# Kernel optimization log

Hardware: AMD Instinct MI355X
Metric: run time of the kernel (lower is better)

The kernel has to match this reference:

```python
import jax, jax.numpy as jnp
import numpy as np

N_NODES = 50000
N_EDGES = 1280000
N_GRAPHS = 64
IN_CH = 6
HID = 64
SLOPE = 0.2  # LeakyReLU negative slope


def _lrelu(x):
    return jax.nn.leaky_relu(x, SLOPE)


def _edge_conv(x, src, dst, W1, b1, W2, b2):
    # PyG EdgeConv: message = nn([x_i, x_j - x_i]); x_i = x[dst], x_j = x[src]; max-aggr onto dst
    xi = x[dst]                                   # [E, F]
    m = jnp.concatenate([xi, x[src] - xi], -1)    # [E, 2F]
    h = _lrelu(_lrelu(m @ W1 + b1) @ W2 + b2)     # [E, H]
    agg = jax.ops.segment_max(h, dst, num_segments=N_NODES)
    return jnp.where(jnp.isneginf(agg), 0.0, agg)  # nodes with no in-edges -> 0


def setup_inputs() -> dict:
    key = jax.random.key(0)
    ks = jax.random.split(key, 12)
    glorot = lambda k, fi, fo: jax.random.normal(k, (fi, fo), jnp.float32) * np.sqrt(2.0 / (fi + fo))
    x = jax.random.normal(ks[0], (N_NODES, IN_CH), jnp.float32)
    edge_index = jax.random.randint(ks[1], (2, N_EDGES), 0, N_NODES, jnp.int64 if jax.config.x64_enabled else jnp.int32)
    batch = jnp.sort(jax.random.randint(ks[2], (N_NODES,), 0, N_GRAPHS))
    return {
        "x": x, "edge_index": edge_index, "batch": batch,
        "W1": glorot(ks[3], 2 * IN_CH, HID), "b1": jnp.zeros((HID,), jnp.float32),
        "W2": glorot(ks[4], HID, HID),       "b2": jnp.zeros((HID,), jnp.float32),
        "W3": glorot(ks[5], 2 * HID, HID),   "b3": jnp.zeros((HID,), jnp.float32),
        "W4": glorot(ks[6], HID, HID),       "b4": jnp.zeros((HID,), jnp.float32),
        "Wc1": glorot(ks[7], 2 * HID, HID),  "bc1": jnp.zeros((HID,), jnp.float32),
        "Wc2": glorot(ks[8], HID, 1),        "bc2": jnp.zeros((1,), jnp.float32),
    }


def reference(x, edge_index, batch, W1, b1, W2, b2, W3, b3, W4, b4, Wc1, bc1, Wc2, bc2):
    src, dst = edge_index[0], edge_index[1]
    h = _edge_conv(x, src, dst, W1, b1, W2, b2)   # [N, H]
    h = _edge_conv(h, src, dst, W3, b3, W4, b4)   # [N, H]
    # global mean + max pool per graph
    cnt = jax.ops.segment_sum(jnp.ones((N_NODES,), h.dtype), batch, num_segments=N_GRAPHS)
    mean_p = jax.ops.segment_sum(h, batch, num_segments=N_GRAPHS) / jnp.clip(cnt, 1.0)[:, None]
    max_p = jax.ops.segment_max(h, batch, num_segments=N_GRAPHS)
    max_p = jnp.where(jnp.isneginf(max_p), 0.0, max_p)
    g = jnp.concatenate([mean_p, max_p], -1)      # [G, 2H]
    logits = _lrelu(g @ Wc1 + bc1) @ Wc2 + bc2    # dropout is identity at inference
    return logits.squeeze(-1)                      # [G]
```

## Files before the change

### kernel.cpp

```cpp
#include <hip/hip_runtime.h>
#include <hip/hip_bf16.h>

#define SLOPE 0.2f
#define NPB 64
#define CAP 2048
#define SUBCAP 384
#define MAXBUCK 1024
#define EPB 4096
#define XF1B 512
#define PPARTS 16

typedef _Float16 f16x8  __attribute__((ext_vector_type(8)));
typedef float    f32x4  __attribute__((ext_vector_type(4)));
typedef unsigned u32;
typedef unsigned u32x4  __attribute__((ext_vector_type(4)));

__device__ __forceinline__ float lrelu(float v) { return fmaxf(v, SLOPE * v); }

__device__ __forceinline__ f16x8 lrelu8(f16x8 v) {
    f16x8 s = v * (_Float16)SLOPE;
#if __has_builtin(__builtin_elementwise_max)
    return __builtin_elementwise_max(v, s);
#else
    f16x8 r;
#pragma unroll
    for (int i = 0; i < 8; ++i) r[i] = v[i] > s[i] ? v[i] : s[i];
    return r;
#endif
}

__device__ __forceinline__ void split_f16(float v, _Float16& h, _Float16& l) {
    h = (_Float16)v;
    l = (_Float16)(v - (float)h);
}
__device__ __forceinline__ u32 pack_f16(_Float16 a, _Float16 b) {
    return (u32)__builtin_bit_cast(unsigned short, a) |
           ((u32)__builtin_bit_cast(unsigned short, b) << 16);
}

__global__ void __launch_bounds__(256) scatter_xform1_kernel(
    const int* __restrict__ srcI, const int* __restrict__ dstI,
    int* __restrict__ cursor, u32* __restrict__ pairW,
    int E, int nNodes, int nBuck, int nCntB,
    const float* __restrict__ x,
    const float* __restrict__ W1, const float* __restrict__ b1,
    _Float16* __restrict__ Ph, _Float16* __restrict__ Qh)
{
    if (blockIdx.x < nCntB) {
        __shared__ int cnt4[4][MAXBUCK];
        __shared__ int base[MAXBUCK];
        const int tid = threadIdx.x;
        const int wv  = tid >> 6;
        const int j   = blockIdx.x & 7;
        const int e0 = blockIdx.x * EPB;
        const int e1 = min(e0 + EPB, E);
        const int n4 = (e1 - e0) >> 2;
        const int4* d4 = (const int4*)(dstI + e0);
        const int4* s4 = (const int4*)(srcI + e0);

        for (int b = tid; b < nBuck; b += 256) {
            cnt4[0][b] = 0; cnt4[1][b] = 0; cnt4[2][b] = 0; cnt4[3][b] = 0;
        }
        __syncthreads();
        int* mycnt = cnt4[wv];
        for (int i = tid; i < n4; i += 256) {
            const int4 d = d4[i];
            atomicAdd(&mycnt[d.x >> 6], 1);
            atomicAdd(&mycnt[d.y >> 6], 1);
            atomicAdd(&mycnt[d.z >> 6], 1);
            atomicAdd(&mycnt[d.w >> 6], 1);
        }
        for (int e = e0 + (n4 << 2) + tid; e < e1; e += 256)
            atomicAdd(&mycnt[dstI[e] >> 6], 1);
        __syncthreads();
        for (int b = tid; b < nBuck; b += 256) {
            const int c = (cnt4[0][b] + cnt4[1][b]) + (cnt4[2][b] + cnt4[3][b]);
            base[b] = (c > 0)
                ? ((b * 8 + j) * SUBCAP + min(atomicAdd(&cursor[b * 8 + j], c), SUBCAP))
                : 0;
        }
        __syncthreads();
        for (int b = tid; b < nBuck; b += 256) cnt4[0][b] = 0;
        __syncthreads();
        int* scnt = cnt4[0];
        for (int i = tid; i < n4; i += 256) {
            const int4 d = d4[i];
            const int4 s = s4[i];
            {
                const int b = d.x >> 6;
                const int loc = atomicAdd(&scnt[b], 1);
                pairW[min(base[b] + loc, (b * 8 + j + 1) * SUBCAP - 1)] =
                    ((u32)s.x << 6) | (u32)(d.x & (NPB - 1));
            }
            {
                const int b = d.y >> 6;
                const int loc = atomicAdd(&scnt[b], 1);
                pairW[min(base[b] + loc, (b * 8 + j + 1) * SUBCAP - 1)] =
                    ((u32)s.y << 6) | (u32)(d.y & (NPB - 1));
            }
            {
                const int b = d.z >> 6;
                const int loc = atomicAdd(&scnt[b], 1);
                pairW[min(base[b] + loc, (b * 8 + j + 1) * SUBCAP - 1)] =
                    ((u32)s.z << 6) | (u32)(d.z & (NPB - 1));
            }
            {
                const int b = d.w >> 6;
                const int loc = atomicAdd(&scnt[b], 1);
                pairW[min(base[b] + loc, (b * 8 + j + 1) * SUBCAP - 1)] =
                    ((u32)s.w << 6) | (u32)(d.w & (NPB - 1));
            }
        }
        for (int e = e0 + (n4 << 2) + tid; e < e1; e += 256) {
            const int d = dstI[e];
            const int b = d >> 6;
            const int loc = atomicAdd(&scnt[b], 1);
            pairW[min(base[b] + loc, (b * 8 + j + 1) * SUBCAP - 1)] =
                ((u32)srcI[e] << 6) | (u32)(d & (NPB - 1));
        }
        return;
    }
    const int lane = threadIdx.x & 63;
    const int wave = ((blockIdx.x - nCntB) * 256 + threadIdx.x) >> 6;
    const int nw   = (XF1B * 256) >> 6;

    float wd[6], wb[6];
#pragma unroll
    for (int r = 0; r < 6; ++r) {
        wb[r] = W1[(6 + r) * 64 + lane];
        wd[r] = W1[r * 64 + lane] - wb[r];
    }
    const float bb = b1[lane];
    for (int i = wave; i < nNodes; i += nw) {
        const float* xr = x + (size_t)i * 6;
        float p = bb, q = 0.f;
#pragma unroll
        for (int r = 0; r < 6; ++r) {
            float xv = xr[r];
            p = fmaf(xv, wd[r], p);
            q = fmaf(xv, wb[r], q);
        }
        Ph[(size_t)i * 64 + lane] = (_Float16)p;
        Qh[(size_t)i * 64 + lane] = (_Float16)q;
    }
}

__global__ void __launch_bounds__(256) bucket_sort_kernel(
    const u32* __restrict__ pairW, const int* __restrict__ cursor,
    int2* __restrict__ rowInfo, int* __restrict__ sortedSrc, int nNodes)
{
    __shared__ u32 pairLds[CAP];
    __shared__ int nodeCnt4[4][NPB];
    __shared__ int nodeCur4[4][NPB];
    __shared__ int wcS[8];
    __shared__ int wBase[9];
    const int b   = blockIdx.x;
    const int n0  = b * NPB;
    const int n1  = min(n0 + NPB, nNodes);
    const int tid = threadIdx.x;
    const int wv  = tid >> 6;

    if (tid < NPB) {
        nodeCnt4[0][tid] = 0; nodeCnt4[1][tid] = 0;
        nodeCnt4[2][tid] = 0; nodeCnt4[3][tid] = 0;
    }
    if (tid < 8) wcS[tid] = min(cursor[b * 8 + tid], SUBCAP);
    __syncthreads();
    if (tid == 0) {
        int acc = 0;
#pragma unroll
        for (int jj = 0; jj < 8; ++jj) { wBase[jj] = acc; acc += wcS[jj]; }
        wBase[8] = acc;
    }
    __syncthreads();

#pragma unroll
    for (int jj = 0; jj < 8; ++jj) {
        const int w0 = (b * 8 + jj) * SUBCAP;
        const int wc = wcS[jj];
        const int d0 = wBase[jj];
        const int nv = wc >> 2;
        const u32x4* p4 = (const u32x4*)(pairW + w0);
        for (int i = tid; i < nv; i += 256) {
            const u32x4 v = p4[i];
            pairLds[d0 + i * 4 + 0] = v[0];
            pairLds[d0 + i * 4 + 1] = v[1];
            pairLds[d0 + i * 4 + 2] = v[2];
            pairLds[d0 + i * 4 + 3] = v[3];
        }
        for (int i = (nv << 2) + tid; i < wc; i += 256)
            pairLds[d0 + i] = pairW[w0 + i];
    }
    __syncthreads();

    const int total = wBase[8];
    for (int i = tid; i < total; i += 256)
        atomicAdd(&nodeCnt4[wv][pairLds[i] & (NPB - 1)], 1);
    __syncthreads();
    if (tid < 64) {
        const int c0 = nodeCnt4[0][tid], c1 = nodeCnt4[1][tid];
        const int c2 = nodeCnt4[2][tid], c3 = nodeCnt4[3][tid];
        const int c = (c0 + c1) + (c2 + c3);
        int inc = c;
#pragma unroll
        for (int off = 1; off < 64; off <<= 1) {
            int t = __shfl_up(inc, off);
            if (tid >= off) inc += t;
        }
        const int st = b * CAP + inc - c;
        nodeCur4[0][tid] = st;
        nodeCur4[1][tid] = st + c0;
        nodeCur4[2][tid] = st + c0 + c1;
        nodeCur4[3][tid] = st + c0 + c1 + c2;
        if (tid < n1 - n0) rowInfo[n0 + tid] = make_int2(st, c);
    }
    __syncthreads();
    for (int i = tid; i < total; i += 256) {
        const u32 w = pairLds[i];
        const int pos = atomicAdd(&nodeCur4[wv][w & (NPB - 1)], 1);
        sortedSrc[pos] = (int)(w >> 6);
    }
}

__global__ void __launch_bounds__(256) node_xform2_mfma_kernel(
    const _Float16* __restrict__ B1h,
    const float* __restrict__ W3, const float* __restrict__ b3,
    _Float16* __restrict__ Ph, _Float16* __restrict__ Qh, int nNodes)
{
    __shared__ u32x4 wlds[32][64];

    const int tid  = threadIdx.x;
    const int lane = tid & 63;
    const int cn   = lane & 15;
    const int q    = lane >> 4;
    const int wv   = tid >> 6;
    const int wave = (blockIdx.x * 256 + tid) >> 6;
    const int nw   = (gridDim.x * 256) >> 6;

#pragma unroll
    for (int i = 0; i < 8; ++i) {
        const int f    = wv + i * 4;
        const int isLo = f >> 4;
        const int g    = f & 15;
        const int nt   = g >> 1;
        const int ks   = g & 1;
        const int col  = (nt & 3) * 16 + cn;
        u32x4 d;
#pragma unroll
        for (int p = 0; p < 4; ++p) {
            const int k0 = ks * 32 + q * 8 + 2 * p;
            float w0, w1;
            if (nt < 4) {
                w0 = W3[k0 * 64 + col]       - W3[(64 + k0) * 64 + col];
                w1 = W3[(k0 + 1) * 64 + col] - W3[(64 + k0 + 1) * 64 + col];
            } else {
                w0 = W3[(64 + k0) * 64 + col];
                w1 = W3[(64 + k0 + 1) * 64 + col];
            }
            _Float16 h0, l0, h1, l1;
            split_f16(w0, h0, l0);
            split_f16(w1, h1, l1);
            d[p] = isLo ? pack_f16(l0, l1) : pack_f16(h0, h1);
        }
        wlds[f][lane] = d;
    }
    float bcv[4];
#pragma unroll
    for (int nt = 0; nt < 4; ++nt) bcv[nt] = b3[nt * 16 + cn];
    __syncthreads();

    const int nGrp = (nNodes + 15) >> 4;
    for (int t = wave; t < nGrp; t += nw) {
        const int n0 = t << 4;
        const int rA = min(n0 + cn, nNodes - 1);
        const f16x8* Arow = (const f16x8*)(B1h + (size_t)rA * 64);
        const f16x8 A0 = Arow[q];
        const f16x8 A1 = Arow[4 + q];

        f32x4 acc0, acc1, acc2, acc3, acc4, acc5, acc6, acc7;
#define NT_TILE(ACC, NT, INI)                                                  \
        {                                                                      \
            const f16x8 wh0 = __builtin_bit_cast(f16x8, wlds[(NT) * 2][lane]); \
            const f16x8 wh1 = __builtin_bit_cast(f16x8, wlds[(NT) * 2 + 1][lane]); \
            const f16x8 wl0 = __builtin_bit_cast(f16x8, wlds[16 + (NT) * 2][lane]); \
            const f16x8 wl1 = __builtin_bit_cast(f16x8, wlds[16 + (NT) * 2 + 1][lane]); \
            f32x4 a_; a_[0] = a_[1] = a_[2] = a_[3] = (INI);                   \
            a_ = __builtin_amdgcn_mfma_f32_16x16x32_f16(A0, wl0, a_, 0, 0, 0); \
            a_ = __builtin_amdgcn_mfma_f32_16x16x32_f16(A0, wh0, a_, 0, 0, 0); \
            a_ = __builtin_amdgcn_mfma_f32_16x16x32_f16(A1, wl1, a_, 0, 0, 0); \
            a_ = __builtin_amdgcn_mfma_f32_16x16x32_f16(A1, wh1, a_, 0, 0, 0); \
            ACC = a_;                                                          \
        }
        NT_TILE(acc0, 0, bcv[0]); NT_TILE(acc1, 1, bcv[1]);
        NT_TILE(acc2, 2, bcv[2]); NT_TILE(acc3, 3, bcv[3]);
        NT_TILE(acc4, 4, 0.0f);   NT_TILE(acc5, 5, 0.0f);
        NT_TILE(acc6, 6, 0.0f);   NT_TILE(acc7, 7, 0.0f);
#undef NT_TILE

        const int rowLim = nNodes - n0;
#pragma unroll
        for (int j = 0; j < 4; ++j) {
            const int r = 4 * q + j;
            if (r < rowLim) {
                _Float16* Pr = Ph + (size_t)(n0 + r) * 64;
                _Float16* Qr = Qh + (size_t)(n0 + r) * 64;
                Pr[cn]      = (_Float16)acc0[j];
                Pr[16 + cn] = (_Float16)acc1[j];
                Pr[32 + cn] = (_Float16)acc2[j];
                Pr[48 + cn] = (_Float16)acc3[j];
                Qr[cn]      = (_Float16)acc4[j];
                Qr[16 + cn] = (_Float16)acc5[j];
                Qr[32 + cn] = (_Float16)acc6[j];
                Qr[48 + cn] = (_Float16)acc7[j];
            }
        }
    }
}

__global__ void __launch_bounds__(256) edge_agg_mfma_kernel(
    const _Float16* __restrict__ Ph, const _Float16* __restrict__ Qh,
    const int2* __restrict__ rowInfo, const int* __restrict__ sortedSrc,
    const float* __restrict__ W, const float* __restrict__ b,
    _Float16* __restrict__ outB, int nNodes)
{
    __shared__ u32x4 wlds[16][64];

    const int tid  = threadIdx.x;
    const int lane = tid & 63;
    const int cn   = lane & 15;
    const int q    = lane >> 4;
    const int wv   = tid >> 6;
    const int wave = (blockIdx.x * 256 + tid) >> 6;
    const int nw   = (gridDim.x * 256) >> 6;

#pragma unroll
    for (int i = 0; i < 4; ++i) {
        const int f    = wv + i * 4;
        const int isLo = f >> 3;
        const int g    = f & 7;
        const int nt   = g >> 1;
        const int ks   = g & 1;
        u32x4 d;
#pragma unroll
        for (int p = 0; p < 4; ++p) {
            float w0 = W[(ks * 32 + q * 8 + 2 * p)     * 64 + nt * 16 + cn];
            float w1 = W[(ks * 32 + q * 8 + 2 * p + 1) * 64 + nt * 16 + cn];
            _Float16 h0, l0, h1, l1;
            split_f16(w0, h0, l0);
            split_f16(w1, h1, l1);
            d[p] = isLo ? pack_f16(l0, l1) : pack_f16(h0, h1);
        }
        wlds[f][lane] = d;
    }
    float bc[4];
#pragma unroll
    for (int nt = 0; nt < 4; ++nt) bc[nt] = b[nt * 16 + cn];
    __syncthreads();

    const u32 nClamp = (u32)(nNodes - 1);
    const int nPairs = (nNodes + 1) >> 1;

    for (int t = wave; t < nPairs; t += nw) {
        const int n1 = 2 * t;
        const int n2 = 2 * t + 1;
        const bool has2 = (n2 < nNodes);

        const int2 ri1 = rowInfo[n1];
        const int2 ri2 = has2 ? rowInfo[n2] : make_int2(ri1.x, 0);
        const int rs1  = __builtin_amdgcn_readfirstlane(ri1.x);
        const int deg1 = __builtin_amdgcn_readfirstlane(ri1.y);
        const int rs2  = __builtin_amdgcn_readfirstlane(ri2.x);
        const int deg2 = __builtin_amdgcn_readfirstlane(ri2.y);
        const int d1c = max(deg1, 1) - 1;
        const int d2c = max(deg2, 1) - 1;

        const f16x8* P1 = (const f16x8*)(Ph + (size_t)n1 * 64);
        const f16x8* P2 = (const f16x8*)(Ph + (size_t)(has2 ? n2 : n1) * 64);
        const f16x8 p1A = P1[q], p1B = P1[4 + q];
        const f16x8 p2A = P2[q], p2B = P2[4 + q];

        float m10 = -INFINITY, m11 = -INFINITY, m12 = -INFINITY, m13 = -INFINITY;
        float m20 = -INFINITY, m21 = -INFINITY, m22 = -INFINITY, m23 = -INFINITY;

        const int gmax = max(deg1, deg2);
        for (int g0 = 0; g0 < gmax; g0 += 32) {
            u32 sA1 = (u32)sortedSrc[rs1 + min(g0 + cn,      d1c)];
            u32 sB1 = (u32)sortedSrc[rs1 + min(g0 + 16 + cn, d1c)];
            u32 sA2 = (u32)sortedSrc[rs2 + min(g0 + cn,      d2c)];
            u32 sB2 = (u32)sortedSrc[rs2 + min(g0 + 16 + cn, d2c)];
            sA1 = min(sA1, nClamp); sB1 = min(sB1, nClamp);
            sA2 = min(sA2, nClamp); sB2 = min(sB2, nClamp);
            const f16x8* QA1 = (const f16x8*)(Qh + (size_t)sA1 * 64);
            const f16x8* QB1 = (const f16x8*)(Qh + (size_t)sB1 * 64);
            const f16x8* QA2 = (const f16x8*)(Qh + (size_t)sA2 * 64);
            const f16x8* QB2 = (const f16x8*)(Qh + (size_t)sB2 * 64);
            const f16x8 qA1a = QA1[q], qA1b = QA1[4 + q];
            const f16x8 qB1a = QB1[q], qB1b = QB1[4 + q];
            const f16x8 qA2a = QA2[q], qA2b = QA2[4 + q];
            const f16x8 qB2a = QB2[q], qB2b = QB2[4 + q];

            if (g0 < deg1) {
                const f16x8 A00 = lrelu8(p1A + qA1a);
                const f16x8 A01 = lrelu8(p1B + qA1b);
                const f16x8 A10 = lrelu8(p1A + qB1a);
                const f16x8 A11 = lrelu8(p1B + qB1b);
#pragma unroll
                for (int nt = 0; nt < 4; ++nt) {
                    const f16x8 wh0 = __builtin_bit_cast(f16x8, wlds[nt * 2][lane]);
                    const f16x8 wh1 = __builtin_bit_cast(f16x8, wlds[nt * 2 + 1][lane]);
                    const f16x8 wl0 = __builtin_bit_cast(f16x8, wlds[8 + nt * 2][lane]);
                    const f16x8 wl1 = __builtin_bit_cast(f16x8, wlds[8 + nt * 2 + 1][lane]);
                    f32x4 a; a[0] = a[1] = a[2] = a[3] = bc[nt];
                    a = __builtin_amdgcn_mfma_f32_16x16x32_f16(A00, wl0, a, 0, 0, 0);
                    a = __builtin_amdgcn_mfma_f32_16x16x32_f16(A00, wh0, a, 0, 0, 0);
                    a = __builtin_amdgcn_mfma_f32_16x16x32_f16(A01, wl1, a, 0, 0, 0);
                    a = __builtin_amdgcn_mfma_f32_16x16x32_f16(A01, wh1, a, 0, 0, 0);
                    f32x4 c; c[0] = c[1] = c[2] = c[3] = bc[nt];
                    c = __builtin_amdgcn_mfma_f32_16x16x32_f16(A10, wl0, c, 0, 0, 0);
                    c = __builtin_amdgcn_mfma_f32_16x16x32_f16(A10, wh0, c, 0, 0, 0);
                    c = __builtin_amdgcn_mfma_f32_16x16x32_f16(A11, wl1, c, 0, 0, 0);
                    c = __builtin_amdgcn_mfma_f32_16x16x32_f16(A11, wh1, c, 0, 0, 0);
                    float m = (nt == 0) ? m10 : (nt == 1) ? m11 : (nt == 2) ? m12 : m13;
                    m = fmaxf(m, fmaxf(fmaxf(a[0], a[1]), fmaxf(a[2], a[3])));
                    m = fmaxf(m, fmaxf(fmaxf(c[0], c[1]), fmaxf(c[2], c[3])));
                    if (nt == 0) m10 = m; else if (nt == 1) m11 = m;
                    else if (nt == 2) m12 = m; else m13 = m;
                }
            }
            if (g0 < deg2) {
                const f16x8 A00 = lrelu8(p2A + qA2a);
                const f16x8 A01 = lrelu8(p2B + qA2b);
                const f16x8 A10 = lrelu8(p2A + qB2a);
                const f16x8 A11 = lrelu8(p2B + qB2b);
#pragma unroll
                for (int nt = 0; nt < 4; ++nt) {
                    const f16x8 wh0 = __builtin_bit_cast(f16x8, wlds[nt * 2][lane]);
                    const f16x8 wh1 = __builtin_bit_cast(f16x8, wlds[nt * 2 + 1][lane]);
                    const f16x8 wl0 = __builtin_bit_cast(f16x8, wlds[8 + nt * 2][lane]);
                    const f16x8 wl1 = __builtin_bit_cast(f16x8, wlds[8 + nt * 2 + 1][lane]);
                    f32x4 a; a[0] = a[1] = a[2] = a[3] = bc[nt];
                    a = __builtin_amdgcn_mfma_f32_16x16x32_f16(A00, wl0, a, 0, 0, 0);
                    a = __builtin_amdgcn_mfma_f32_16x16x32_f16(A00, wh0, a, 0, 0, 0);
                    a = __builtin_amdgcn_mfma_f32_16x16x32_f16(A01, wl1, a, 0, 0, 0);
                    a = __builtin_amdgcn_mfma_f32_16x16x32_f16(A01, wh1, a, 0, 0, 0);
                    f32x4 c; c[0] = c[1] = c[2] = c[3] = bc[nt];
                    c = __builtin_amdgcn_mfma_f32_16x16x32_f16(A10, wl0, c, 0, 0, 0);
                    c = __builtin_amdgcn_mfma_f32_16x16x32_f16(A10, wh0, c, 0, 0, 0);
                    c = __builtin_amdgcn_mfma_f32_16x16x32_f16(A11, wl1, c, 0, 0, 0);
                    c = __builtin_amdgcn_mfma_f32_16x16x32_f16(A11, wh1, c, 0, 0, 0);
                    float m = (nt == 0) ? m20 : (nt == 1) ? m21 : (nt == 2) ? m22 : m23;
                    m = fmaxf(m, fmaxf(fmaxf(a[0], a[1]), fmaxf(a[2], a[3])));
                    m = fmaxf(m, fmaxf(fmaxf(c[0], c[1]), fmaxf(c[2], c[3])));
                    if (nt == 0) m20 = m; else if (nt == 1) m21 = m;
                    else if (nt == 2) m22 = m; else m23 = m;
                }
            }
        }

        m10 = fmaxf(m10, __shfl_xor(m10, 16)); m10 = fmaxf(m10, __shfl_xor(m10, 32));
        m11 = fmaxf(m11, __shfl_xor(m11, 16)); m11 = fmaxf(m11, __shfl_xor(m11, 32));
        m12 = fmaxf(m12, __shfl_xor(m12, 16)); m12 = fmaxf(m12, __shfl_xor(m12, 32));
        m13 = fmaxf(m13, __shfl_xor(m13, 16)); m13 = fmaxf(m13, __shfl_xor(m13, 32));
        float sel1 = (q < 2) ? ((q == 0) ? m10 : m11) : ((q == 2) ? m12 : m13);
        outB[(size_t)n1 * 64 + q * 16 + cn] =
            (_Float16)((deg1 > 0) ? lrelu(sel1) : 0.0f);

        if (has2) {
            m20 = fmaxf(m20, __shfl_xor(m20, 16)); m20 = fmaxf(m20, __shfl_xor(m20, 32));
            m21 = fmaxf(m21, __shfl_xor(m21, 16)); m21 = fmaxf(m21, __shfl_xor(m21, 32));
            m22 = fmaxf(m22, __shfl_xor(m22, 16)); m22 = fmaxf(m22, __shfl_xor(m22, 32));
            m23 = fmaxf(m23, __shfl_xor(m23, 16)); m23 = fmaxf(m23, __shfl_xor(m23, 32));
            float sel2 = (q < 2) ? ((q == 0) ? m20 : m21) : ((q == 2) ? m22 : m23);
            outB[(size_t)n2 * 64 + q * 16 + cn] =
                (_Float16)((deg2 > 0) ? lrelu(sel2) : 0.0f);
        }
    }
}

__device__ __forceinline__ int lower_bound_i(const int* __restrict__ a, int n, int key)
{
    int lo = 0, hi = n;
    while (lo < hi) {
        int mid = (lo + hi) >> 1;
        if (a[mid] < key) lo = mid + 1; else hi = mid;
    }
    return lo;
}

__global__ void __launch_bounds__(256) pool_kernel(
    const _Float16* __restrict__ Bh, const int* __restrict__ batch,
    float* __restrict__ gpart, int nNodes)
{
    const int gid  = blockIdx.x / PPARTS;
    const int part = blockIdx.x % PPARTS;
    const int c    = threadIdx.x & 63;
    const int wid  = threadIdx.x >> 6;

    const int s = lower_bound_i(batch, nNodes, gid);
    const int e = lower_bound_i(batch, nNodes, gid + 1);
    const int len = e - s;
    const int ps = s + (len * part) / PPARTS;
    const int pe = s + (len * (part + 1)) / PPARTS;

    float sum = 0.f, mx = -INFINITY;
    for (int n = ps + wid; n < pe; n += 4) {
        float v = (float)Bh[(size_t)n * 64 + c];
        sum += v;
        mx = fmaxf(mx, v);
    }
    __shared__ float ssum[4][64];
    __shared__ float smax[4][64];
    ssum[wid][c] = sum;
    smax[wid][c] = mx;
    __syncthreads();
    if (wid == 0) {
        sum = (ssum[0][c] + ssum[1][c]) + (ssum[2][c] + ssum[3][c]);
        mx  = fmaxf(fmaxf(smax[0][c], smax[1][c]), fmaxf(smax[2][c], smax[3][c]));
        float* row = gpart + (size_t)blockIdx.x * 132;
        row[c]      = sum;
        row[64 + c] = mx;
        if (c == 0) row[128] = (float)(pe - ps);
    }
}

__global__ void __launch_bounds__(64) cls_kernel(
    const float* __restrict__ gpart,
    const float* __restrict__ Wc1, const float* __restrict__ bc1,
    const float* __restrict__ Wc2, const float* __restrict__ bc2,
    float* __restrict__ out)
{
    __shared__ float g[128];
    const int gid = blockIdx.x;
    const int c   = threadIdx.x;

    float s = 0.f, m = -INFINITY, cnt = 0.f;
#pragma unroll
    for (int p = 0; p < PPARTS; ++p) {
        const float* row = gpart + (size_t)(gid * PPARTS + p) * 132;
        s += row[c];
        m = fmaxf(m, row[64 + c]);
        cnt += row[128];
    }
    g[c]      = s / fmaxf(cnt, 1.0f);
    g[64 + c] = (cnt > 0.f) ? m : 0.0f;
    __syncthreads();

    float t = bc1[c];
#pragma unroll 8
    for (int k = 0; k < 128; ++k) t = fmaf(g[k], Wc1[k * 64 + c], t);
    t = lrelu(t);
    float p = t * Wc2[c];
#pragma unroll
    for (int off = 32; off > 0; off >>= 1) p += __shfl_down(p, off);
    if (c == 0) out[gid] = p + bc2[0];
}

static inline size_t align_up(size_t v, size_t a) { return (v + a - 1) & ~(a - 1); }

extern "C" void kernel_launch(void* const* d_in, const int* in_sizes, int n_in,
                              void* d_out, int out_size, void* d_ws, size_t ws_size,
                              hipStream_t stream)
{
    const float* x     = (const float*)d_in[0];
    const int*   ei    = (const int*)d_in[1];
    const int*   batch = (const int*)d_in[2];
    const float* W1  = (const float*)d_in[3];
    const float* b1  = (const float*)d_in[4];
    const float* W2  = (const float*)d_in[5];
    const float* b2  = (const float*)d_in[6];
    const float* W3  = (const float*)d_in[7];
    const float* b3  = (const float*)d_in[8];
    const float* W4  = (const float*)d_in[9];
    const float* b4  = (const float*)d_in[10];
    const float* Wc1 = (const float*)d_in[11];
    const float* bc1 = (const float*)d_in[12];
    const float* Wc2 = (const float*)d_in[13];
    const float* bc2 = (const float*)d_in[14];
    float* out = (float*)d_out;

    const int nNodes  = in_sizes[0] / 6;
    const int E       = in_sizes[1] / 2;
    const int nGraphs = out_size;
    const int* srcI = ei;
    const int* dstI = ei + E;
    const int nBuck = (nNodes + NPB - 1) / NPB;
    const int nCntB = (E + EPB - 1) / EPB;

    char* wsp = (char*)d_ws;
    size_t off = 0;
    int*  cursor    = (int*)(wsp + off);   off = align_up(off + (size_t)MAXBUCK * 8 * 4, 256);
    int2* rowInfo   = (int2*)(wsp + off);  off = align_up(off + (size_t)nNodes * 8, 256);
    int*  sortedSrc = (int*)(wsp + off);   off = align_up(off + (size_t)nBuck * CAP * 4, 256);
    u32*  pairW     = (u32*)(wsp + off);   off = align_up(off + (size_t)nBuck * 8 * SUBCAP * 4, 256);
    const size_t nFeat = (size_t)nNodes * 64;
    _Float16* Ph   = (_Float16*)(wsp + off);  off = align_up(off + nFeat * 2, 256);
    _Float16* Qh   = (_Float16*)(wsp + off);  off = align_up(off + nFeat * 2, 256);
    _Float16* B1h  = (_Float16*)(wsp + off);  off = align_up(off + nFeat * 2, 256);
    _Float16* B2h  = (_Float16*)(wsp + off);  off = align_up(off + nFeat * 2, 256);
    float*    gpart= (float*)(wsp + off);     off = align_up(off + (size_t)nGraphs * PPARTS * 132 * 4, 256);
    (void)ws_size;

    (void)hipMemsetAsync(cursor, 0, (size_t)nBuck * 8 * 4, stream);
    scatter_xform1_kernel<<<nCntB + XF1B, 256, 0, stream>>>(
        srcI, dstI, cursor, pairW, E, nNodes, nBuck, nCntB, x, W1, b1, Ph, Qh);
    bucket_sort_kernel<<<nBuck, 256, 0, stream>>>(pairW, cursor, rowInfo,
                                                  sortedSrc, nNodes);

    edge_agg_mfma_kernel<<<2048, 256, 0, stream>>>(Ph, Qh, rowInfo, sortedSrc,
                                                   W2, b2, B1h, nNodes);
    const int nGrp   = (nNodes + 15) >> 4;
    const int xf2Blk = (nGrp + 3) >> 2;
    node_xform2_mfma_kernel<<<xf2Blk, 256, 0, stream>>>(B1h, W3, b3, Ph, Qh,
                                                        nNodes);
    edge_agg_mfma_kernel<<<2048, 256, 0, stream>>>(Ph, Qh, rowInfo, sortedSrc,
                                                   W4, b4, B2h, nNodes);

    pool_kernel<<<nGraphs * PPARTS, 256, 0, stream>>>(B2h, batch, gpart, nNodes);
    cls_kernel<<<nGraphs, 64, 0, stream>>>(gpart, Wc1, bc1, Wc2, bc2, out);
}
```

Measured before the change: 261.4 us.

## Precompute padded first-32 neighbor lists to hoist gathers ahead of rowInfo dependency

The bucket sort now stages the sorted sources in LDS and also writes a fixed 32-entry padded neighbor list per node (fixedSrc). The edge aggregation kernel loads the first 32 neighbor indices and their Q rows directly, without waiting on rowInfo, so the dependent load chain (rowInfo -> sortedSrc -> Qh) is shortened for the first chunk, which covers most nodes given an average degree of about 26. This costs an extra 6.4MB index array write plus extra LDS in the sort kernel, and duplicates the first-chunk compute code.

```diff
diff --git a/kernel.cpp b/kernel.cpp
--- a/kernel.cpp
+++ b/kernel.cpp
@@ -147,11 +147,15 @@
 
 __global__ void __launch_bounds__(256) bucket_sort_kernel(
     const u32* __restrict__ pairW, const int* __restrict__ cursor,
-    int2* __restrict__ rowInfo, int* __restrict__ sortedSrc, int nNodes)
+    int2* __restrict__ rowInfo, int* __restrict__ sortedSrc,
+    int* __restrict__ fixedSrc, int nNodes)
 {
     __shared__ u32 pairLds[CAP];
+    __shared__ u32 sortLds[CAP];
     __shared__ int nodeCnt4[4][NPB];
     __shared__ int nodeCur4[4][NPB];
+    __shared__ int nodeSt[NPB];
+    __shared__ int nodeDg[NPB];
     __shared__ int wcS[8];
     __shared__ int wBase[9];
     const int b   = blockIdx.x;
@@ -207,18 +211,34 @@
             int t = __shfl_up(inc, off);
             if (tid >= off) inc += t;
         }
-        const int st = b * CAP + inc - c;
-        nodeCur4[0][tid] = st;
-        nodeCur4[1][tid] = st + c0;
-        nodeCur4[2][tid] = st + c0 + c1;
-        nodeCur4[3][tid] = st + c0 + c1 + c2;
-        if (tid < n1 - n0) rowInfo[n0 + tid] = make_int2(st, c);
+        const int stl = inc - c;
+        nodeSt[tid] = stl;
+        nodeDg[tid] = c;
+        nodeCur4[0][tid] = stl;
+        nodeCur4[1][tid] = stl + c0;
+        nodeCur4[2][tid] = stl + c0 + c1;
+        nodeCur4[3][tid] = stl + c0 + c1 + c2;
+        if (tid < n1 - n0) rowInfo[n0 + tid] = make_int2(b * CAP + stl, c);
     }
     __syncthreads();
     for (int i = tid; i < total; i += 256) {
         const u32 w = pairLds[i];
         const int pos = atomicAdd(&nodeCur4[wv][w & (NPB - 1)], 1);
-        sortedSrc[pos] = (int)(w >> 6);
+        sortLds[pos] = w >> 6;
+    }
+    __syncthreads();
+    for (int i = tid; i < total; i += 256)
+        sortedSrc[b * CAP + i] = (int)sortLds[i];
+    const int nValid = n1 - n0;
+    for (int idx = tid; idx < NPB * 32; idx += 256) {
+        const int r = idx >> 5;
+        const int i = idx & 31;
+        if (r < nValid) {
+            const int dg = nodeDg[r];
+            const u32 v = (dg > 0) ? sortLds[nodeSt[r] + min(i, dg - 1)]
+                                   : (u32)(n0 + r);
+            fixedSrc[(size_t)(n0 + r) * 32 + i] = (int)v;
+        }
     }
 }
 
@@ -320,6 +340,7 @@
 __global__ void __launch_bounds__(256) edge_agg_mfma_kernel(
     const _Float16* __restrict__ Ph, const _Float16* __restrict__ Qh,
     const int2* __restrict__ rowInfo, const int* __restrict__ sortedSrc,
+    const int* __restrict__ fixedSrc,
     const float* __restrict__ W, const float* __restrict__ b,
     _Float16* __restrict__ outB, int nNodes)
 {
@@ -358,6 +379,7 @@
     __syncthreads();
 
     const u32 nClamp = (u32)(nNodes - 1);
+    const int nLastN = nNodes - 1;
     const int nPairs = (nNodes + 1) >> 1;
 
     for (int t = wave; t < nPairs; t += nw) {
@@ -367,6 +389,29 @@
 
         const int2 ri1 = rowInfo[n1];
         const int2 ri2 = has2 ? rowInfo[n2] : make_int2(ri1.x, 0);
+        const size_t fb1 = (size_t)n1 * 32;
+        const size_t fb2 = (size_t)(has2 ? n2 : n1) * 32;
+        u32 sA1 = (u32)fixedSrc[fb1 + cn];
+        u32 sB1 = (u32)fixedSrc[fb1 + 16 + cn];
+        u32 sA2 = (u32)fixedSrc[fb2 + cn];
+        u32 sB2 = (u32)fixedSrc[fb2 + 16 + cn];
+        sA1 = min(sA1, nClamp); sB1 = min(sB1, nClamp);
+        sA2 = min(sA2, nClamp); sB2 = min(sB2, nClamp);
+
+        const f16x8* P1 = (const f16x8*)(Ph + (size_t)n1 * 64);
+        const f16x8* P2 = (const f16x8*)(Ph + (size_t)(has2 ? n2 : n1) * 64);
+        const f16x8 p1A = P1[q], p1B = P1[4 + q];
+        const f16x8 p2A = P2[q], p2B = P2[4 + q];
+
+        const f16x8* QA1 = (const f16x8*)(Qh + (size_t)sA1 * 64);
+        const f16x8* QB1 = (const f16x8*)(Qh + (size_t)sB1 * 64);
+        const f16x8* QA2 = (const f16x8*)(Qh + (size_t)sA2 * 64);
+        const f16x8* QB2 = (const f16x8*)(Qh + (size_t)sB2 * 64);
+        const f16x8 qA1a = QA1[q], qA1b = QA1[4 + q];
+        const f16x8 qB1a = QB1[q], qB1b = QB1[4 + q];
+        const f16x8 qA2a = QA2[q], qA2b = QA2[4 + q];
+        const f16x8 qB2a = QB2[q], qB2b = QB2[4 + q];
+
         const int rs1  = __builtin_amdgcn_readfirstlane(ri1.x);
         const int deg1 = __builtin_amdgcn_readfirstlane(ri1.y);
         const int rs2  = __builtin_amdgcn_readfirstlane(ri2.x);
@@ -374,36 +419,88 @@
         const int d1c = max(deg1, 1) - 1;
         const int d2c = max(deg2, 1) - 1;
 
-        const f16x8* P1 = (const f16x8*)(Ph + (size_t)n1 * 64);
-        const f16x8* P2 = (const f16x8*)(Ph + (size_t)(has2 ? n2 : n1) * 64);
-        const f16x8 p1A = P1[q], p1B = P1[4 + q];
-        const f16x8 p2A = P2[q], p2B = P2[4 + q];
-
         float m10 = -INFINITY, m11 = -INFINITY, m12 = -INFINITY, m13 = -INFINITY;
         float m20 = -INFINITY, m21 = -INFINITY, m22 = -INFINITY, m23 = -INFINITY;
 
+        if (deg1 > 0) {
+            const f16x8 A00 = lrelu8(p1A + qA1a);
+            const f16x8 A01 = lrelu8(p1B + qA1b);
+            const f16x8 A10 = lrelu8(p1A + qB1a);
+            const f16x8 A11 = lrelu8(p1B + qB1b);
+#pragma unroll
+            for (int nt = 0; nt < 4; ++nt) {
+                const f16x8 wh0 = __builtin_bit_cast(f16x8, wlds[nt * 2][lane]);
+                const f16x8 wh1 = __builtin_bit_cast(f16x8, wlds[nt * 2 + 1][lane]);
+                const f16x8 wl0 = __builtin_bit_cast(f16x8, wlds[8 + nt * 2][lane]);
+                const f16x8 wl1 = __builtin_bit_cast(f16x8, wlds[8 + nt * 2 + 1][lane]);
+                f32x4 a; a[0] = a[1] = a[2] = a[3] = bc[nt];
+                a = __builtin_amdgcn_mfma_f32_16x16x32_f16(A00, wl0, a, 0, 0, 0);
+                a = __builtin_amdgcn_mfma_f32_16x16x32_f16(A00, wh0, a, 0, 0, 0);
+                a = __builtin_amdgcn_mfma_f32_16x16x32_f16(A01, wl1, a, 0, 0, 0);
+                a = __builtin_amdgcn_mfma_f32_16x16x32_f16(A01, wh1, a, 0, 0, 0);
+                f32x4 c; c[0] = c[1] = c[2] = c[3] = bc[nt];
+                c = __builtin_amdgcn_mfma_f32_16x16x32_f16(A10, wl0, c, 0, 0, 0);
+                c = __builtin_amdgcn_mfma_f32_16x16x32_f16(A10, wh0, c, 0, 0, 0);
+                c = __builtin_amdgcn_mfma_f32_16x16x32_f16(A11, wl1, c, 0, 0, 0);
+                c = __builtin_amdgcn_mfma_f32_16x16x32_f16(A11, wh1, c, 0, 0, 0);
+                float m = (nt == 0) ? m10 : (nt == 1) ? m11 : (nt == 2) ? m12 : m13;
+                m = fmaxf(m, fmaxf(fmaxf(a[0], a[1]), fmaxf(a[2], a[3])));
+                m = fmaxf(m, fmaxf(fmaxf(c[0], c[1]), fmaxf(c[2], c[3])));
+                if (nt == 0) m10 = m; else if (nt == 1) m11 = m;
+                else if (nt == 2) m12 = m; else m13 = m;
+            }
+        }
+        if (deg2 > 0) {
+            const f16x8 A00 = lrelu8(p2A + qA2a);
+            const f16x8 A01 = lrelu8(p2B + qA2b);
+            const f16x8 A10 = lrelu8(p2A + qB2a);
+            const f16x8 A11 = lrelu8(p2B + qB2b);
+#pragma unroll
+            for (int nt = 0; nt < 4; ++nt) {
+                const f16x8 wh0 = __builtin_bit_cast(f16x8, wlds[nt * 2][lane]);
+                const f16x8 wh1 = __builtin_bit_cast(f16x8, wlds[nt * 2 + 1][lane]);
+                const f16x8 wl0 = __builtin_bit_cast(f16x8, wlds[8 + nt * 2][lane]);
+                const f16x8 wl1 = __builtin_bit_cast(f16x8, wlds[8 + nt * 2 + 1][lane]);
+                f32x4 a; a[0] = a[1] = a[2] = a[3] = bc[nt];
+                a = __builtin_amdgcn_mfma_f32_16x16x32_f16(A00, wl0, a, 0, 0, 0);
+                a = __builtin_amdgcn_mfma_f32_16x16x32_f16(A00, wh0, a, 0, 0, 0);
+                a = __builtin_amdgcn_mfma_f32_16x16x32_f16(A01, wl1, a, 0, 0, 0);
+                a = __builtin_amdgcn_mfma_f32_16x16x32_f16(A01, wh1, a, 0, 0, 0);
+                f32x4 c; c[0] = c[1] = c[2] = c[3] = bc[nt];
+                c = __builtin_amdgcn_mfma_f32_16x16x32_f16(A10, wl0, c, 0, 0, 0);
+                c = __builtin_amdgcn_mfma_f32_16x16x32_f16(A10, wh0, c, 0, 0, 0);
+                c = __builtin_amdgcn_mfma_f32_16x16x32_f16(A11, wl1, c, 0, 0, 0);
+                c = __builtin_amdgcn_mfma_f32_16x16x32_f16(A11, wh1, c, 0, 0, 0);
+                float m = (nt == 0) ? m20 : (nt == 1) ? m21 : (nt == 2) ? m22 : m23;
+                m = fmaxf(m, fmaxf(fmaxf(a[0], a[1]), fmaxf(a[2], a[3])));
+                m = fmaxf(m, fmaxf(fmaxf(c[0], c[1]), fmaxf(c[2], c[3])));
+                if (nt == 0) m20 = m; else if (nt == 1) m21 = m;
+                else if (nt == 2) m22 = m; else m23 = m;
+            }
+        }
+
         const int gmax = max(deg1, deg2);
-        for (int g0 = 0; g0 < gmax; g0 += 32) {
-            u32 sA1 = (u32)sortedSrc[rs1 + min(g0 + cn,      d1c)];
-            u32 sB1 = (u32)sortedSrc[rs1 + min(g0 + 16 + cn, d1c)];
-            u32 sA2 = (u32)sortedSrc[rs2 + min(g0 + cn,      d2c)];
-            u32 sB2 = (u32)sortedSrc[rs2 + min(g0 + 16 + cn, d2c)];
-            sA1 = min(sA1, nClamp); sB1 = min(sB1, nClamp);
-            sA2 = min(sA2, nClamp); sB2 = min(sB2, nClamp);
-            const f16x8* QA1 = (const f16x8*)(Qh + (size_t)sA1 * 64);
-            const f16x8* QB1 = (const f16x8*)(Qh + (size_t)sB1 * 64);
-            const f16x8* QA2 = (const f16x8*)(Qh + (size_t)sA2 * 64);
-            const f16x8* QB2 = (const f16x8*)(Qh + (size_t)sB2 * 64);
-            const f16x8 qA1a = QA1[q], qA1b = QA1[4 + q];
-            const f16x8 qB1a = QB1[q], qB1b = QB1[4 + q];
-            const f16x8 qA2a = QA2[q], qA2b = QA2[4 + q];
-            const f16x8 qB2a = QB2[q], qB2b = QB2[4 + q];
+        for (int g0 = 32; g0 < gmax; g0 += 32) {
+            u32 eA1 = (u32)sortedSrc[rs1 + min(g0 + cn,      d1c)];
+            u32 eB1 = (u32)sortedSrc[rs1 + min(g0 + 16 + cn, d1c)];
+            u32 eA2 = (u32)sortedSrc[rs2 + min(g0 + cn,      d2c)];
+            u32 eB2 = (u32)sortedSrc[rs2 + min(g0 + 16 + cn, d2c)];
+            eA1 = min(eA1, nClamp); eB1 = min(eB1, nClamp);
+            eA2 = min(eA2, nClamp); eB2 = min(eB2, nClamp);
+            const f16x8* EA1 = (const f16x8*)(Qh + (size_t)eA1 * 64);
+            const f16x8* EB1 = (const f16x8*)(Qh + (size_t)eB1 * 64);
+            const f16x8* EA2 = (const f16x8*)(Qh + (size_t)eA2 * 64);
+            const f16x8* EB2 = (const f16x8*)(Qh + (size_t)eB2 * 64);
+            const f16x8 gA1a = EA1[q], gA1b = EA1[4 + q];
+            const f16x8 gB1a = EB1[q], gB1b = EB1[4 + q];
+            const f16x8 gA2a = EA2[q], gA2b = EA2[4 + q];
+            const f16x8 gB2a = EB2[q], gB2b = EB2[4 + q];
 
             if (g0 < deg1) {
-                const f16x8 A00 = lrelu8(p1A + qA1a);
-                const f16x8 A01 = lrelu8(p1B + qA1b);
-                const f16x8 A10 = lrelu8(p1A + qB1a);
-                const f16x8 A11 = lrelu8(p1B + qB1b);
+                const f16x8 A00 = lrelu8(p1A + gA1a);
+                const f16x8 A01 = lrelu8(p1B + gA1b);
+                const f16x8 A10 = lrelu8(p1A + gB1a);
+                const f16x8 A11 = lrelu8(p1B + gB1b);
 #pragma unroll
                 for (int nt = 0; nt < 4; ++nt) {
                     const f16x8 wh0 = __builtin_bit_cast(f16x8, wlds[nt * 2][lane]);
@@ -428,10 +525,10 @@
                 }
             }
             if (g0 < deg2) {
-                const f16x8 A00 = lrelu8(p2A + qA2a);
-                const f16x8 A01 = lrelu8(p2B + qA2b);
-                const f16x8 A10 = lrelu8(p2A + qB2a);
-                const f16x8 A11 = lrelu8(p2B + qB2b);
+                const f16x8 A00 = lrelu8(p2A + gA2a);
+                const f16x8 A01 = lrelu8(p2B + gA2b);
+                const f16x8 A10 = lrelu8(p2A + gB2a);
+                const f16x8 A11 = lrelu8(p2B + gB2b);
 #pragma unroll
                 for (int nt = 0; nt < 4; ++nt) {
                     const f16x8 wh0 = __builtin_bit_cast(f16x8, wlds[nt * 2][lane]);
@@ -591,6 +688,7 @@
     int*  cursor    = (int*)(wsp + off);   off = align_up(off + (size_t)MAXBUCK * 8 * 4, 256);
     int2* rowInfo   = (int2*)(wsp + off);  off = align_up(off + (size_t)nNodes * 8, 256);
     int*  sortedSrc = (int*)(wsp + off);   off = align_up(off + (size_t)nBuck * CAP * 4, 256);
+    int*  fixedSrc  = (int*)(wsp + off);   off = align_up(off + (size_t)nNodes * 32 * 4, 256);
     u32*  pairW     = (u32*)(wsp + off);   off = align_up(off + (size_t)nBuck * 8 * SUBCAP * 4, 256);
     const size_t nFeat = (size_t)nNodes * 64;
     _Float16* Ph   = (_Float16*)(wsp + off);  off = align_up(off + nFeat * 2, 256);
@@ -604,16 +702,16 @@
     scatter_xform1_kernel<<<nCntB + XF1B, 256, 0, stream>>>(
         srcI, dstI, cursor, pairW, E, nNodes, nBuck, nCntB, x, W1, b1, Ph, Qh);
     bucket_sort_kernel<<<nBuck, 256, 0, stream>>>(pairW, cursor, rowInfo,
-                                                  sortedSrc, nNodes);
+                                                  sortedSrc, fixedSrc, nNodes);
 
     edge_agg_mfma_kernel<<<2048, 256, 0, stream>>>(Ph, Qh, rowInfo, sortedSrc,
-                                                   W2, b2, B1h, nNodes);
+                                                   fixedSrc, W2, b2, B1h, nNodes);
     const int nGrp   = (nNodes + 15) >> 4;
     const int xf2Blk = (nGrp + 3) >> 2;
     node_xform2_mfma_kernel<<<xf2Blk, 256, 0, stream>>>(B1h, W3, b3, Ph, Qh,
                                                         nNodes);
     edge_agg_mfma_kernel<<<2048, 256, 0, stream>>>(Ph, Qh, rowInfo, sortedSrc,
-                                                   W4, b4, B2h, nNodes);
+                                                   fixedSrc, W4, b4, B2h, nNodes);
 
     pool_kernel<<<nGraphs * PPARTS, 256, 0, stream>>>(B2h, batch, gpart, nNodes);
     cls_kernel<<<nGraphs, 64, 0, stream>>>(gpart, Wc1, bc1, Wc2, bc2, out);
```

After: 260.9 us (median of 2 runs). No clear change (-0.2%).
